# Optimization experiments

Hardware: AMD Instinct MI355X
Metric: run time of the kernel (lower is better)

## Reference

```python
import jax, jax.numpy as jnp
import numpy as np

B, T, C, H = 2, 2048, 1024, 16
D = C // H  # head dim = 64
EPS = 1e-5


def _layernorm(x, g, b):
    mu = jnp.mean(x, axis=-1, keepdims=True)
    var = jnp.mean((x - mu) ** 2, axis=-1, keepdims=True)
    return (x - mu) * jax.lax.rsqrt(var + EPS) * g + b


def setup_inputs() -> dict:
    key = jax.random.key(0)
    ks = jax.random.split(key, 16)
    s = 1.0 / np.sqrt(C)
    inp = {
        "x": jax.random.normal(ks[0], (B, T, C), dtype=jnp.float32),
        "Wq": jax.random.normal(ks[1], (C, C), dtype=jnp.float32) * s,
        "bq": jnp.zeros((C,), jnp.float32),
        "Wk": jax.random.normal(ks[2], (C, C), dtype=jnp.float32) * s,
        "bk": jnp.zeros((C,), jnp.float32),
        "Wv": jax.random.normal(ks[3], (C, C), dtype=jnp.float32) * s,
        "bv": jnp.zeros((C,), jnp.float32),
        "Wo": jax.random.normal(ks[4], (C, C), dtype=jnp.float32) * s,
        "bo": jnp.zeros((C,), jnp.float32),
        "ln1_g": jnp.ones((C,), jnp.float32),
        "ln1_b": jnp.zeros((C,), jnp.float32),
        "ln2_g": jnp.ones((C,), jnp.float32),
        "ln2_b": jnp.zeros((C,), jnp.float32),
        "W1": jax.random.normal(ks[5], (C, 4 * C), dtype=jnp.float32) * s,
        "b1": jnp.zeros((4 * C,), jnp.float32),
        "W2": jax.random.normal(ks[6], (4 * C, C), dtype=jnp.float32) * (1.0 / np.sqrt(4 * C)),
        "b2": jnp.zeros((C,), jnp.float32),
    }
    return inp


def _block(x, Wq, bq, Wk, bk, Wv, bv, Wo, bo, ln1_g, ln1_b, ln2_g, ln2_b, W1, b1, W2, b2):
    # --- attention sublayer (pre-LN, residual) ---
    h = _layernorm(x, ln1_g, ln1_b)
    q = (h @ Wq + bq).reshape(B, T, H, D)
    k = (h @ Wk + bk).reshape(B, T, H, D)
    v = (h @ Wv + bv).reshape(B, T, H, D)
    scores = jnp.einsum("bthd,bshd->bhts", q, k) * (1.0 / np.sqrt(D))
    attn = jax.nn.softmax(scores, axis=-1)  # dropout is identity at eval
    y = jnp.einsum("bhts,bshd->bthd", attn, v).reshape(B, T, C)
    x = x + (y @ Wo + bo)
    # --- MLP sublayer (pre-LN, residual) ---
    h2 = _layernorm(x, ln2_g, ln2_b)
    m = jax.nn.gelu(h2 @ W1 + b1, approximate=False)  # torch nn.GELU() is exact erf
    x = x + (m @ W2 + b2)
    return x


def reference(x, Wq, bq, Wk, bk, Wv, bv, Wo, bo, ln1_g, ln1_b, ln2_g, ln2_b, W1, b1, W2, b2):
    return _block(x, Wq, bq, Wk, bk, Wv, bv, Wo, bo, ln1_g, ln1_b, ln2_g, ln2_b, W1, b1, W2, b2)
```

## Files before the change

kernel.cpp:

```cpp
#include <hip/hip_runtime.h>
#include <math.h>

typedef unsigned short u16;
typedef unsigned int   u32;
using bf16x8 = __attribute__((ext_vector_type(8))) short;
using f32x4  = __attribute__((ext_vector_type(4))) float;
using f32x16 = __attribute__((ext_vector_type(16))) float;

static constexpr int Bb = 2, Tt = 2048, Cc = 1024, Hh = 16, Dd = 64;
static constexpr int QS = 3072;
static constexpr float QSCALE = 0.125f * 1.44269504089f;

__device__ __forceinline__ u16 f2bf(float f){
  u32 u = __builtin_bit_cast(u32, f);
  u += 0x7fffu + ((u >> 16) & 1u);
  return (u16)(u >> 16);
}
__device__ __forceinline__ float bf2f(u16 v){
  u32 u = (u32)v << 16;
  return __builtin_bit_cast(float, u);
}

__device__ __forceinline__ void gl2lds16(const void* g, void* l){
  __builtin_amdgcn_global_load_lds((const __attribute__((address_space(1))) void*)g,
                                   (__attribute__((address_space(3))) void*)l, 16, 0, 0);
}

template<int N> __device__ __forceinline__ void waitvm(){
  if constexpr (N == 0) asm volatile("s_waitcnt vmcnt(0)" ::: "memory");
  else if constexpr (N == 4) asm volatile("s_waitcnt vmcnt(4)" ::: "memory");
  else if constexpr (N == 6) asm volatile("s_waitcnt vmcnt(6)" ::: "memory");
  else if constexpr (N == 8) asm volatile("s_waitcnt vmcnt(8)" ::: "memory");
}

__device__ __forceinline__ void barrier_pin(){
  __builtin_amdgcn_s_barrier();
  __builtin_amdgcn_sched_barrier(0);
}

__device__ __forceinline__ f32x4 mfma16(bf16x8 a, bf16x8 b, f32x4 c){
  return __builtin_amdgcn_mfma_f32_16x16x32_bf16(a, b, c, 0, 0, 0);
}
__device__ __forceinline__ f32x16 mfma32(bf16x8 a, bf16x8 b, f32x16 c){
  return __builtin_amdgcn_mfma_f32_32x32x16_bf16(a, b, c, 0, 0, 0);
}

__device__ __forceinline__ float exp2f_fast(float x){
#if __has_builtin(__builtin_amdgcn_exp2f)
  return __builtin_amdgcn_exp2f(x);
#else
  return __expf(x * 0.69314718056f);
#endif
}

__device__ __forceinline__ float gelu_f(float x){
  return 0.5f * x * (1.0f + erff(x * 0.70710678118654752f));
}

__device__ __forceinline__ void plane_swap(u32& a, u32& b){
  asm("v_permlane32_swap_b32 %0, %1" : "+v"(a), "+v"(b));
}
__device__ __forceinline__ u32 cvtpk_bf16(float lo, float hi){
  u32 r;
  asm("v_cvt_pk_bf16_f32 %0, %1, %2" : "=v"(r) : "v"(lo), "v"(hi));
  return r;
}

__device__ __forceinline__ bf16x8 ldlds(const u16* p){ return *(const bf16x8*)p; }

__global__ __launch_bounds__(256) void ln_kernel(const float* __restrict__ x,
    const float* __restrict__ g, const float* __restrict__ b, u16* __restrict__ out)
{
  int row = blockIdx.x;
  int tid = threadIdx.x;
  const float4* xr = (const float4*)(x + (size_t)row * Cc);
  float4 v = xr[tid];
  float s  = v.x + v.y + v.z + v.w;
  float s2 = v.x*v.x + v.y*v.y + v.z*v.z + v.w*v.w;
  #pragma unroll
  for (int off = 1; off < 64; off <<= 1){ s += __shfl_xor(s, off); s2 += __shfl_xor(s2, off); }
  __shared__ float red[8];
  int wid = tid >> 6;
  if ((tid & 63) == 0){ red[wid] = s; red[4 + wid] = s2; }
  __syncthreads();
  s  = red[0] + red[1] + red[2] + red[3];
  s2 = red[4] + red[5] + red[6] + red[7];
  float mu   = s * (1.0f / Cc);
  float var  = s2 * (1.0f / Cc) - mu * mu;
  float rstd = rsqrtf(var + 1e-5f);
  const float4 gg = ((const float4*)g)[tid];
  const float4 bb = ((const float4*)b)[tid];
  ushort4 o;
  o.x = f2bf((v.x - mu) * rstd * gg.x + bb.x);
  o.y = f2bf((v.y - mu) * rstd * gg.y + bb.y);
  o.z = f2bf((v.z - mu) * rstd * gg.z + bb.z);
  o.w = f2bf((v.w - mu) * rstd * gg.w + bb.w);
  *(ushort4*)(out + (size_t)row * Cc + tid * 4) = o;
}

__global__ __launch_bounds__(256) void transpose_cast_kernel(const float* __restrict__ in,
    u16* __restrict__ out, int R, int Ccols)
{
  __shared__ float tile[32][33];
  int tx = threadIdx.x, ty = threadIdx.y;
  int c0 = blockIdx.x * 32, r0 = blockIdx.y * 32;
  #pragma unroll
  for (int j = 0; j < 4; j++) tile[ty + j*8][tx] = in[(size_t)(r0 + ty + j*8) * Ccols + c0 + tx];
  __syncthreads();
  #pragma unroll
  for (int j = 0; j < 4; j++) out[(size_t)(c0 + ty + j*8) * R + r0 + tx] = f2bf(tile[tx][ty + j*8]);
}

__global__ __launch_bounds__(256) void transpose4_kernel(
    const float* __restrict__ s0, const float* __restrict__ s1,
    const float* __restrict__ s2, const float* __restrict__ s3,
    u16* __restrict__ d0, u16* __restrict__ d1, u16* __restrict__ d2, u16* __restrict__ d3)
{
  __shared__ float tile[32][33];
  int z = blockIdx.z;
  const float* in = (z == 0) ? s0 : (z == 1) ? s1 : (z == 2) ? s2 : s3;
  u16* out        = (z == 0) ? d0 : (z == 1) ? d1 : (z == 2) ? d2 : d3;
  int tx = threadIdx.x, ty = threadIdx.y;
  int c0 = blockIdx.x * 32, r0 = blockIdx.y * 32;
  #pragma unroll
  for (int j = 0; j < 4; j++) tile[ty + j*8][tx] = in[(size_t)(r0 + ty + j*8) * 1024 + c0 + tx];
  __syncthreads();
  #pragma unroll
  for (int j = 0; j < 4; j++) out[(size_t)(c0 + ty + j*8) * 1024 + r0 + tx] = f2bf(tile[tx][ty + j*8]);
}

__global__ __launch_bounds__(256) void pack3_kernel(const float* __restrict__ a,
    const float* __restrict__ b, const float* __restrict__ c, float* __restrict__ o)
{
  int i = blockIdx.x * 256 + threadIdx.x;
  float v = (i < 1024) ? a[i] : (i < 2048 ? b[i - 1024] : c[i - 2048]);
  o[i] = v;
}

__global__ __launch_bounds__(256) void transpose_v_kernel(const u16* __restrict__ v, u16* __restrict__ vt)
{
  __shared__ u16 tile[32][33];
  int tx = threadIdx.x, ty = threadIdx.y;
  int bh = blockIdx.z; int b = bh >> 4, h = bh & 15;
  int t0 = blockIdx.x * 32, d0 = blockIdx.y * 32;
  const u16* src = v + (size_t)b * Tt * QS + h * Dd;
  #pragma unroll
  for (int j = 0; j < 4; j++) tile[ty + j*8][tx] = src[(size_t)(t0 + ty + j*8) * QS + d0 + tx];
  __syncthreads();
  u16* dst = vt + (size_t)bh * Dd * Tt;
  #pragma unroll
  for (int j = 0; j < 4; j++) dst[(size_t)(d0 + ty + j*8) * Tt + t0 + tx] = tile[tx][ty + j*8];
}

template<int EPI>
__global__ __launch_bounds__(256, 4) void gemm32_kernel(
    const u16* __restrict__ A, const u16* __restrict__ BT,
    const float* __restrict__ bias, void* __restrict__ out,
    int K, int ldA, int ldOut)
{
  __shared__ alignas(16) u16 As[2][128 * 32];
  __shared__ alignas(16) u16 Bs[2][128 * 32];

  const int tid  = threadIdx.x;
  const int lane = tid & 63, wid = tid >> 6;
  const int l15  = lane & 15, lg = lane >> 4;

  const int gx  = gridDim.x;
  const int lin = blockIdx.x + gx * blockIdx.y;
  const int nwg = gx * gridDim.y;
  const int wl  = (lin & 7) * (nwg >> 3) + (lin >> 3);
  const int rowBase = (wl % gx) * 128, colBase = (wl / gx) * 128;

  const int wr = wid >> 1, wc = wid & 1;

  f32x4 acc[4][4] = {};

  const int g0 = tid, g1 = tid + 256;
  const int r0 = g0 >> 2, w0 = (g0 & 3) ^ ((r0 >> 1) & 3);
  const int r1 = g1 >> 2, w1 = (g1 & 3) ^ ((r1 >> 1) & 3);
  const u16* pA0 = A  + (size_t)(rowBase + r0) * ldA + w0 * 8;
  const u16* pA1 = A  + (size_t)(rowBase + r1) * ldA + w1 * 8;
  const u16* pB0 = BT + (size_t)(colBase + r0) * K   + w0 * 8;
  const u16* pB1 = BT + (size_t)(colBase + r1) * K   + w1 * 8;
  const u32 d0 = (u32)g0 * 8, d1 = (u32)g1 * 8;

  u32 oa[4], ob[4];
  #pragma unroll
  for (int mi = 0; mi < 4; mi++){
    int r = wr * 64 + mi * 16 + l15;
    oa[mi] = (u32)(r * 32 + ((lg ^ ((r >> 1) & 3)) << 3));
  }
  #pragma unroll
  for (int ni = 0; ni < 4; ni++){
    int r = wc * 64 + ni * 16 + l15;
    ob[ni] = (u32)(r * 32 + ((lg ^ ((r >> 1) & 3)) << 3));
  }

  gl2lds16(pA0, &As[0][d0]); gl2lds16(pA1, &As[0][d1]);
  gl2lds16(pB0, &Bs[0][d0]); gl2lds16(pB1, &Bs[0][d1]);
  pA0 += 32; pA1 += 32; pB0 += 32; pB1 += 32;

  const int nt = K >> 5;
  #pragma unroll 2
  for (int t = 0; t < nt - 1; ++t){
    const int cur = t & 1, nxt = cur ^ 1;
    gl2lds16(pA0, &As[nxt][d0]); gl2lds16(pA1, &As[nxt][d1]);
    gl2lds16(pB0, &Bs[nxt][d0]); gl2lds16(pB1, &Bs[nxt][d1]);
    pA0 += 32; pA1 += 32; pB0 += 32; pB1 += 32;
    waitvm<4>();
    __builtin_amdgcn_s_barrier();
    __builtin_amdgcn_sched_barrier(0);

    bf16x8 afr[4], bfr[4];
    #pragma unroll
    for (int mi = 0; mi < 4; mi++) afr[mi] = ldlds(&As[cur][oa[mi]]);
    #pragma unroll
    for (int ni = 0; ni < 4; ni++) bfr[ni] = ldlds(&Bs[cur][ob[ni]]);
    __builtin_amdgcn_s_setprio(1);
    #pragma unroll
    for (int mi = 0; mi < 4; mi++)
      #pragma unroll
      for (int ni = 0; ni < 4; ni++)
        acc[mi][ni] = mfma16(afr[mi], bfr[ni], acc[mi][ni]);
    __builtin_amdgcn_s_setprio(0);

    __builtin_amdgcn_sched_barrier(0);
    __builtin_amdgcn_s_barrier();
  }
  {
    const int cur = (nt - 1) & 1;
    waitvm<0>();
    __builtin_amdgcn_s_barrier();
    bf16x8 afr[4], bfr[4];
    #pragma unroll
    for (int mi = 0; mi < 4; mi++) afr[mi] = ldlds(&As[cur][oa[mi]]);
    #pragma unroll
    for (int ni = 0; ni < 4; ni++) bfr[ni] = ldlds(&Bs[cur][ob[ni]]);
    #pragma unroll
    for (int mi = 0; mi < 4; mi++)
      #pragma unroll
      for (int ni = 0; ni < 4; ni++)
        acc[mi][ni] = mfma16(afr[mi], bfr[ni], acc[mi][ni]);
  }

  #pragma unroll
  for (int mi = 0; mi < 4; mi++){
    #pragma unroll
    for (int ni = 0; ni < 4; ni++){
      int row = rowBase + wr * 64 + mi * 16 + lg * 4;
      int col = colBase + wc * 64 + ni * 16 + l15;
      float bc = bias[col];
      #pragma unroll
      for (int r = 0; r < 4; r++){
        float val = acc[mi][ni][r] + bc;
        size_t idx = (size_t)(row + r) * ldOut + col;
        if constexpr (EPI == 2) ((u16*)out)[idx] = f2bf(gelu_f(val));
        else                    ((u16*)out)[idx] = f2bf(col < 1024 ? val * QSCALE : val);
      }
    }
  }
}

template<int BM, int BN, int WPEU, int EPI>
__global__ __launch_bounds__(256, WPEU) void gemmc_kernel(
    const u16* __restrict__ A, const u16* __restrict__ BT,
    const float* __restrict__ bias, const float* __restrict__ resid,
    void* __restrict__ out, int K, int ldA, int ldOut)
{
  constexpr int MF = BM / 2 / 16;
  constexpr int NF = BN / 2 / 16;
  constexpr int AG = BM / 32;
  constexpr int BG = BN / 32;
  constexpr int NLOADS = AG + BG;

  __shared__ alignas(16) u16 As[2][BM * 64];
  __shared__ alignas(16) u16 Bs[2][BN * 64];

  const int tid  = threadIdx.x;
  const int lane = tid & 63, wid = tid >> 6;
  const int l15  = lane & 15, lg = lane >> 4;

  const int gx  = gridDim.x;
  const int lin = blockIdx.x + gx * blockIdx.y;
  const int nwg = gx * gridDim.y;
  const int wl  = (lin & 7) * (nwg >> 3) + (lin >> 3);
  const int rowBase = (wl % gx) * BM, colBase = (wl / gx) * BN;

  const int wr = wid >> 1, wc = wid & 1;

  f32x4 acc[MF][NF] = {};

  const u16* pA[AG];
  const u16* pB[BG];
  u32 dA[AG], dB[BG];
  #pragma unroll
  for (int j = 0; j < AG; j++){
    int g = tid + 256 * j;
    int r = g >> 3, w = (g & 7) ^ (r & 7);
    pA[j] = A + (size_t)(rowBase + r) * ldA + w * 8;
    dA[j] = (u32)g * 8;
  }
  #pragma unroll
  for (int j = 0; j < BG; j++){
    int g = tid + 256 * j;
    int r = g >> 3, w = (g & 7) ^ (r & 7);
    pB[j] = BT + (size_t)(colBase + r) * K + w * 8;
    dB[j] = (u32)g * 8;
  }

  u32 oa[MF][2], ob[NF][2];
  #pragma unroll
  for (int mi = 0; mi < MF; mi++){
    int r = wr * (BM / 2) + mi * 16 + l15;
    oa[mi][0] = (u32)(r * 64 + ((lg       ^ (r & 7)) << 3));
    oa[mi][1] = (u32)(r * 64 + (((4 + lg) ^ (r & 7)) << 3));
  }
  #pragma unroll
  for (int ni = 0; ni < NF; ni++){
    int r = wc * (BN / 2) + ni * 16 + l15;
    ob[ni][0] = (u32)(r * 64 + ((lg       ^ (r & 7)) << 3));
    ob[ni][1] = (u32)(r * 64 + (((4 + lg) ^ (r & 7)) << 3));
  }

  #pragma unroll
  for (int j = 0; j < AG; j++){ gl2lds16(pA[j], &As[0][dA[j]]); pA[j] += 64; }
  #pragma unroll
  for (int j = 0; j < BG; j++){ gl2lds16(pB[j], &Bs[0][dB[j]]); pB[j] += 64; }

  const int nt = K >> 6;
  #pragma unroll 2
  for (int t = 0; t < nt - 1; ++t){
    const int cur = t & 1, nxt = cur ^ 1;
    #pragma unroll
    for (int j = 0; j < AG; j++){ gl2lds16(pA[j], &As[nxt][dA[j]]); pA[j] += 64; }
    #pragma unroll
    for (int j = 0; j < BG; j++){ gl2lds16(pB[j], &Bs[nxt][dB[j]]); pB[j] += 64; }
    waitvm<NLOADS>();
    __builtin_amdgcn_s_barrier();
    __builtin_amdgcn_sched_barrier(0);

    bf16x8 afr[MF][2], bfr[NF][2];
    #pragma unroll
    for (int mi = 0; mi < MF; mi++){
      afr[mi][0] = ldlds(&As[cur][oa[mi][0]]);
      afr[mi][1] = ldlds(&As[cur][oa[mi][1]]);
    }
    #pragma unroll
    for (int ni = 0; ni < NF; ni++){
      bfr[ni][0] = ldlds(&Bs[cur][ob[ni][0]]);
      bfr[ni][1] = ldlds(&Bs[cur][ob[ni][1]]);
    }
    __builtin_amdgcn_s_setprio(1);
    #pragma unroll
    for (int mi = 0; mi < MF; mi++)
      #pragma unroll
      for (int ni = 0; ni < NF; ni++){
        acc[mi][ni] = mfma16(afr[mi][0], bfr[ni][0], acc[mi][ni]);
        acc[mi][ni] = mfma16(afr[mi][1], bfr[ni][1], acc[mi][ni]);
      }
    __builtin_amdgcn_s_setprio(0);

    __builtin_amdgcn_sched_barrier(0);
    __builtin_amdgcn_s_barrier();
  }
  {
    const int cur = (nt - 1) & 1;
    waitvm<0>();
    __builtin_amdgcn_s_barrier();
    bf16x8 afr[MF][2], bfr[NF][2];
    #pragma unroll
    for (int mi = 0; mi < MF; mi++){
      afr[mi][0] = ldlds(&As[cur][oa[mi][0]]);
      afr[mi][1] = ldlds(&As[cur][oa[mi][1]]);
    }
    #pragma unroll
    for (int ni = 0; ni < NF; ni++){
      bfr[ni][0] = ldlds(&Bs[cur][ob[ni][0]]);
      bfr[ni][1] = ldlds(&Bs[cur][ob[ni][1]]);
    }
    #pragma unroll
    for (int mi = 0; mi < MF; mi++)
      #pragma unroll
      for (int ni = 0; ni < NF; ni++){
        acc[mi][ni] = mfma16(afr[mi][0], bfr[ni][0], acc[mi][ni]);
        acc[mi][ni] = mfma16(afr[mi][1], bfr[ni][1], acc[mi][ni]);
      }
  }

  #pragma unroll
  for (int mi = 0; mi < MF; mi++){
    #pragma unroll
    for (int ni = 0; ni < NF; ni++){
      int row = rowBase + wr * (BM / 2) + mi * 16 + lg * 4;
      int col = colBase + wc * (BN / 2) + ni * 16 + l15;
      float bc = bias[col];
      #pragma unroll
      for (int r = 0; r < 4; r++){
        float val = acc[mi][ni][r] + bc;
        size_t idx = (size_t)(row + r) * ldOut + col;
        if constexpr (EPI == 1) ((float*)out)[idx] = val + resid[idx];
        else                    ((u16*)out)[idx]   = f2bf(val);
      }
    }
  }
}

__global__ __launch_bounds__(256, 4) void attn_kernel(const u16* __restrict__ q, const u16* __restrict__ k,
    const u16* __restrict__ vt, u16* __restrict__ opart, float* __restrict__ ml)
{
  __shared__ alignas(16) u16 Ks[2][64 * 64];
  __shared__ alignas(16) u16 Vs[2][64 * 64];
  int tid  = threadIdx.x;
  int lane = tid & 63, wid = tid >> 6;
  int l31  = lane & 31, hi = lane >> 5;

  int lin = blockIdx.x + 16 * blockIdx.y;
  int wl  = (lin & 7) * 64 + (lin >> 3);
  int qt  = wl & 15, bh = wl >> 4;
  int b = bh >> 4, h = bh & 15;
  int split = blockIdx.z;
  int kt0 = split * (Tt / 2);

  int qglob = qt * 128 + wid * 32 + l31;

  const u16* qp = q + ((size_t)b * Tt + qglob) * QS + h * Dd + hi * 8;
  bf16x8 qf[4];
  #pragma unroll
  for (int s = 0; s < 4; s++) qf[s] = *(const bf16x8*)(qp + s * 16);

  const u16* kbase = k  + (size_t)b * Tt * QS + h * Dd;
  const u16* vbase = vt + (size_t)bh * Dd * Tt;

  f32x16 yacc[2] = {};
  float m2 = -1e30f, lsum = 0.f;

  int g0 = tid, g1 = tid + 256;
  int r0 = g0 >> 3, cb0 = (g0 & 7) ^ (r0 & 7);
  int r1 = g1 >> 3, cb1 = (g1 & 7) ^ (r1 & 7);

  auto stageKV = [&](int buf, int kt){
    gl2lds16(kbase + (size_t)(kt + r0) * QS + cb0 * 8, (u16*)Ks[buf] + wid * 512);
    gl2lds16(kbase + (size_t)(kt + r1) * QS + cb1 * 8, (u16*)Ks[buf] + 2048 + wid * 512);
    gl2lds16(vbase + (size_t)r0 * Tt + kt + cb0 * 8,   (u16*)Vs[buf] + wid * 512);
    gl2lds16(vbase + (size_t)r1 * Tt + kt + cb1 * 8,   (u16*)Vs[buf] + 2048 + wid * 512);
  };

  stageKV(0, kt0);
  int cur = 0;
  for (int kt = kt0; kt < kt0 + Tt / 2; kt += 64) {
    if (kt + 64 < kt0 + Tt / 2) { stageKV(cur ^ 1, kt + 64); waitvm<4>(); }
    else                        { waitvm<0>(); }
    barrier_pin();

    const u16* Ksb = (const u16*)Ks[cur];
    const u16* Vsb = (const u16*)Vs[cur];
    int rx = l31 & 7;

    f32x16 st[2] = {};
    __builtin_amdgcn_s_setprio(1);
    #pragma unroll
    for (int nb = 0; nb < 2; nb++){
      const u16* krow = Ksb + (nb * 32 + l31) * 64;
      #pragma unroll
      for (int s = 0; s < 4; s++){
        bf16x8 kf = *(const bf16x8*)(krow + (((s * 2 + hi) ^ rx) << 3));
        st[nb] = mfma32(kf, qf[s], st[nb]);
      }
    }
    __builtin_amdgcn_s_setprio(0);

    float tm[16];
    #pragma unroll
    for (int i = 0; i < 16; i++) tm[i] = fmaxf(st[0][i], st[1][i]);
    #pragma unroll
    for (int w = 8; w; w >>= 1)
      #pragma unroll
      for (int i = 0; i < w; i++) tm[i] = fmaxf(tm[i], tm[i + w]);
    u32 ma = __builtin_bit_cast(u32, tm[0]), mb = ma;
    plane_swap(ma, mb);
    float mx = fmaxf(__builtin_bit_cast(float, ma), __builtin_bit_cast(float, mb));

    float mnew = fmaxf(m2, mx);
    float alpha = exp2f_fast(m2 - mnew);
    m2 = mnew;

    #pragma unroll
    for (int nb = 0; nb < 2; nb++)
      #pragma unroll
      for (int i = 0; i < 16; i++)
        st[nb][i] = exp2f_fast(st[nb][i] - m2);

    float ts[16];
    #pragma unroll
    for (int i = 0; i < 16; i++) ts[i] = st[0][i] + st[1][i];
    #pragma unroll
    for (int w = 8; w; w >>= 1)
      #pragma unroll
      for (int i = 0; i < w; i++) ts[i] += ts[i + w];
    u32 sa = __builtin_bit_cast(u32, ts[0]), sb = sa;
    plane_swap(sa, sb);
    lsum = lsum * alpha + __builtin_bit_cast(float, sa) + __builtin_bit_cast(float, sb);

    #pragma unroll
    for (int nd = 0; nd < 2; nd++)
      #pragma unroll
      for (int i = 0; i < 16; i++) yacc[nd][i] *= alpha;

    bf16x8 pb[4];
    #pragma unroll
    for (int nb = 0; nb < 2; nb++){
      u32 c[8];
      #pragma unroll
      for (int i = 0; i < 8; i++) c[i] = cvtpk_bf16(st[nb][2 * i], st[nb][2 * i + 1]);
      plane_swap(c[0], c[2]); plane_swap(c[1], c[3]);
      plane_swap(c[4], c[6]); plane_swap(c[5], c[7]);
      u32 f0[4] = {c[0], c[1], c[2], c[3]};
      u32 f1[4] = {c[4], c[5], c[6], c[7]};
      pb[nb * 2 + 0] = *(bf16x8*)f0;
      pb[nb * 2 + 1] = *(bf16x8*)f1;
    }

    __builtin_amdgcn_s_setprio(1);
    #pragma unroll
    for (int nd = 0; nd < 2; nd++){
      const u16* vrow = Vsb + (nd * 32 + l31) * 64;
      #pragma unroll
      for (int ks = 0; ks < 4; ks++){
        bf16x8 vf = *(const bf16x8*)(vrow + (((ks * 2 + hi) ^ rx) << 3));
        yacc[nd] = mfma32(vf, pb[ks], yacc[nd]);
      }
    }
    __builtin_amdgcn_s_setprio(0);

    __builtin_amdgcn_sched_barrier(0);
    barrier_pin();
    cur ^= 1;
  }

  float inv = 1.0f / lsum;
  u16* op = opart + ((size_t)split * (Bb * Tt) + (size_t)b * Tt + qglob) * Cc + h * Dd;
  #pragma unroll
  for (int nd = 0; nd < 2; nd++){
    #pragma unroll
    for (int g = 0; g < 4; g++){
      ushort4 o;
      o.x = f2bf(yacc[nd][g * 4 + 0] * inv);
      o.y = f2bf(yacc[nd][g * 4 + 1] * inv);
      o.z = f2bf(yacc[nd][g * 4 + 2] * inv);
      o.w = f2bf(yacc[nd][g * 4 + 3] * inv);
      *(ushort4*)(op + nd * 32 + g * 8 + hi * 4) = o;
    }
  }
  if (hi == 0){
    float* mlp = ml + (((size_t)split * (Bb * Tt) + (size_t)b * Tt + qglob) * Hh + h) * 2;
    mlp[0] = m2; mlp[1] = lsum;
  }
}

__global__ __launch_bounds__(256) void combine_kernel(const u16* __restrict__ opart,
    const float* __restrict__ ml, u16* __restrict__ y)
{
  int row = blockIdx.x;
  int d0  = threadIdx.x * 4;
  int h   = d0 >> 6;
  const float* p0 = ml + ((size_t)row * Hh + h) * 2;
  const float* p1 = ml + (((size_t)(Bb * Tt) + row) * Hh + h) * 2;
  float m0 = p0[0], l0 = p0[1], m1 = p1[0], l1 = p1[1];
  float M  = fmaxf(m0, m1);
  float u0 = l0 * exp2f_fast(m0 - M), u1 = l1 * exp2f_fast(m1 - M);
  float inv = 1.0f / (u0 + u1);
  float w0 = u0 * inv, w1 = u1 * inv;
  ushort4 a = *(const ushort4*)(opart + (size_t)row * Cc + d0);
  ushort4 c = *(const ushort4*)(opart + ((size_t)(Bb * Tt) + row) * Cc + d0);
  ushort4 o;
  o.x = f2bf(bf2f(a.x) * w0 + bf2f(c.x) * w1);
  o.y = f2bf(bf2f(a.y) * w0 + bf2f(c.y) * w1);
  o.z = f2bf(bf2f(a.z) * w0 + bf2f(c.z) * w1);
  o.w = f2bf(bf2f(a.w) * w0 + bf2f(c.w) * w1);
  *(ushort4*)(y + (size_t)row * Cc + d0) = o;
}

extern "C" void kernel_launch(void* const* d_in, const int* in_sizes, int n_in,
                              void* d_out, int out_size, void* d_ws, size_t ws_size,
                              hipStream_t stream)
{
  (void)in_sizes; (void)n_in; (void)out_size; (void)ws_size;
  const float* x    = (const float*)d_in[0];
  const float* Wq   = (const float*)d_in[1];
  const float* bq   = (const float*)d_in[2];
  const float* Wk   = (const float*)d_in[3];
  const float* bk   = (const float*)d_in[4];
  const float* Wv   = (const float*)d_in[5];
  const float* bv   = (const float*)d_in[6];
  const float* Wo   = (const float*)d_in[7];
  const float* bo   = (const float*)d_in[8];
  const float* ln1g = (const float*)d_in[9];
  const float* ln1b = (const float*)d_in[10];
  const float* ln2g = (const float*)d_in[11];
  const float* ln2b = (const float*)d_in[12];
  const float* W1   = (const float*)d_in[13];
  const float* b1   = (const float*)d_in[14];
  const float* W2   = (const float*)d_in[15];
  const float* b2   = (const float*)d_in[16];

  char* ws = (char*)d_ws;
  const size_t MB = 1024 * 1024;
  u16*   wqkvt = (u16*)(ws + 0 * MB);
  u16*   wot   = (u16*)(ws + 6 * MB);
  u16*   w1t   = (u16*)(ws + 8 * MB);
  u16*   w2t   = (u16*)(ws + 16 * MB);
  float* bqkv  = (float*)(ws + 24 * MB);
  u16*   hbuf  = (u16*)(ws + 25 * MB);
  u16*   qkv   = (u16*)(ws + 33 * MB);
  u16*   vtb   = (u16*)(ws + 57 * MB);
  u16*   yb    = (u16*)(ws + 65 * MB);
  u16*   opart = (u16*)(ws + 73 * MB);
  float* x2    = (float*)(ws + 73 * MB);
  float* mlb   = (float*)(ws + 89 * MB);
  u16*   h2    = hbuf;
  u16*   mb    = qkv;

  dim3 tb(32, 8);
  transpose4_kernel<<<dim3(32, 32, 4), tb, 0, stream>>>(Wq, Wk, Wv, Wo,
      wqkvt, wqkvt + 1024 * 1024, wqkvt + 2048 * 1024, wot);
  transpose_cast_kernel<<<dim3(128, 32), tb, 0, stream>>>(W1, w1t, 1024, 4096);
  transpose_cast_kernel<<<dim3(32, 128), tb, 0, stream>>>(W2, w2t, 4096, 1024);
  pack3_kernel<<<12, 256, 0, stream>>>(bq, bk, bv, bqkv);

  ln_kernel<<<4096, 256, 0, stream>>>(x, ln1g, ln1b, hbuf);

  gemm32_kernel<3><<<dim3(32, 24), 256, 0, stream>>>(hbuf, wqkvt, bqkv, qkv, 1024, 1024, 3072);

  transpose_v_kernel<<<dim3(64, 2, 32), tb, 0, stream>>>(qkv + 2048, vtb);

  attn_kernel<<<dim3(16, 32, 2), 256, 0, stream>>>(qkv, qkv + 1024, vtb, opart, mlb);
  combine_kernel<<<4096, 256, 0, stream>>>(opart, mlb, yb);

  gemmc_kernel<64, 64, 4, 1><<<dim3(64, 16), 256, 0, stream>>>(yb, wot, bo, x, x2, 1024, 1024, 1024);

  ln_kernel<<<4096, 256, 0, stream>>>(x2, ln2g, ln2b, h2);

  gemm32_kernel<2><<<dim3(32, 32), 256, 0, stream>>>(h2, w1t, b1, mb, 1024, 1024, 4096);

  gemmc_kernel<64, 64, 4, 1><<<dim3(64, 16), 256, 0, stream>>>(mb, w2t, b2, x2, (float*)d_out, 4096, 4096, 1024);
}
```

Baseline: 246.6 us.

## Use lazy rescaling, MFMA row-sum and max3 reduction in attention softmax

Restructures the flash-attention softmax inner loop in three ways. The row max is now reduced with three-input max chains. The output and row-sum rescale is skipped unless some lane's max grows by more than 8 (log2 units). The row sum is taken from an extra MFMA of a ones vector against the bf16 probabilities instead of a VALU add tree plus a lane swap. This is meant to cut VALU work in the softmax critical path, at the cost of four extra MFMAs per tile, a wave-wide branch, and a row sum computed from bf16-rounded probabilities, which changes numerics slightly.

```diff
diff --git a/kernel.cpp b/kernel.cpp
--- a/kernel.cpp
+++ b/kernel.cpp
@@ -55,6 +55,10 @@
 
 __device__ __forceinline__ float gelu_f(float x){
   return 0.5f * x * (1.0f + erff(x * 0.70710678118654752f));
+}
+
+__device__ __forceinline__ float fmax3(float a, float b, float c){
+  return fmaxf(fmaxf(a, b), c);
 }
 
 __device__ __forceinline__ void plane_swap(u32& a, u32& b){
@@ -428,6 +432,10 @@
   #pragma unroll
   for (int s = 0; s < 4; s++) qf[s] = *(const bf16x8*)(qp + s * 16);
 
+  bf16x8 ones;
+  #pragma unroll
+  for (int i = 0; i < 8; i++) ones[i] = (short)0x3F80;
+
   const u16* kbase = k  + (size_t)b * Tt * QS + h * Dd;
   const u16* vbase = vt + (size_t)bh * Dd * Tt;
 
@@ -469,42 +477,40 @@
     }
     __builtin_amdgcn_s_setprio(0);
 
-    float tm[16];
-    #pragma unroll
-    for (int i = 0; i < 16; i++) tm[i] = fmaxf(st[0][i], st[1][i]);
-    #pragma unroll
-    for (int w = 8; w; w >>= 1)
-      #pragma unroll
-      for (int i = 0; i < w; i++) tm[i] = fmaxf(tm[i], tm[i + w]);
-    u32 ma = __builtin_bit_cast(u32, tm[0]), mb = ma;
+    float lv[11];
+    #pragma unroll
+    for (int i = 0; i < 10; i++){
+      float e0 = (3*i   < 16) ? st[0][3*i  ] : st[1][3*i  -16];
+      float e1 = (3*i+1 < 16) ? st[0][3*i+1] : st[1][3*i+1-16];
+      float e2 = (3*i+2 < 16) ? st[0][3*i+2] : st[1][3*i+2-16];
+      lv[i] = fmax3(e0, e1, e2);
+    }
+    lv[10] = fmaxf(st[1][14], st[1][15]);
+    float q0 = fmax3(lv[0], lv[1], lv[2]);
+    float q1 = fmax3(lv[3], lv[4], lv[5]);
+    float q2 = fmax3(lv[6], lv[7], lv[8]);
+    float q3 = fmaxf(lv[9], lv[10]);
+    float mloc = fmax3(q0, q1, fmaxf(q2, q3));
+    u32 ma = __builtin_bit_cast(u32, mloc), mb = ma;
     plane_swap(ma, mb);
     float mx = fmaxf(__builtin_bit_cast(float, ma), __builtin_bit_cast(float, mb));
 
-    float mnew = fmaxf(m2, mx);
-    float alpha = exp2f_fast(m2 - mnew);
-    m2 = mnew;
+    if (__any(mx > m2 + 8.0f)){
+      float mnew = fmaxf(m2, mx);
+      float alpha = exp2f_fast(m2 - mnew);
+      m2 = mnew;
+      lsum *= alpha;
+      #pragma unroll
+      for (int nd = 0; nd < 2; nd++)
+        #pragma unroll
+        for (int i = 0; i < 16; i++) yacc[nd][i] *= alpha;
+    }
 
     #pragma unroll
     for (int nb = 0; nb < 2; nb++)
       #pragma unroll
       for (int i = 0; i < 16; i++)
         st[nb][i] = exp2f_fast(st[nb][i] - m2);
-
-    float ts[16];
-    #pragma unroll
-    for (int i = 0; i < 16; i++) ts[i] = st[0][i] + st[1][i];
-    #pragma unroll
-    for (int w = 8; w; w >>= 1)
-      #pragma unroll
-      for (int i = 0; i < w; i++) ts[i] += ts[i + w];
-    u32 sa = __builtin_bit_cast(u32, ts[0]), sb = sa;
-    plane_swap(sa, sb);
-    lsum = lsum * alpha + __builtin_bit_cast(float, sa) + __builtin_bit_cast(float, sb);
-
-    #pragma unroll
-    for (int nd = 0; nd < 2; nd++)
-      #pragma unroll
-      for (int i = 0; i < 16; i++) yacc[nd][i] *= alpha;
 
     bf16x8 pb[4];
     #pragma unroll
@@ -520,7 +526,10 @@
       pb[nb * 2 + 1] = *(bf16x8*)f1;
     }
 
+    f32x16 sacc = {};
     __builtin_amdgcn_s_setprio(1);
+    #pragma unroll
+    for (int ks = 0; ks < 4; ks++) sacc = mfma32(ones, pb[ks], sacc);
     #pragma unroll
     for (int nd = 0; nd < 2; nd++){
       const u16* vrow = Vsb + (nd * 32 + l31) * 64;
@@ -531,6 +540,7 @@
       }
     }
     __builtin_amdgcn_s_setprio(0);
+    lsum += sacc[0];
 
     __builtin_amdgcn_sched_barrier(0);
     barrier_pin();
```

After: 242.8 us. About the same (-1.5%).
